# Kernel tuning notes

Measured on AMD Instinct MI355X. Metric: run time of the kernel, lower is better.

Reference implementation:

```python
import jax, jax.numpy as jnp
import numpy as np

ALPHA = 0.25
GAMMA = 2.0


def _calc_iou(a, b):
    # a: [A,4] anchors (y1,x1,y2,x2); b: [M,4] boxes (x1,y1,x2,y2)
    area = (b[:, 2] - b[:, 0]) * (b[:, 3] - b[:, 1])  # [M]
    iw = jnp.minimum(a[:, 3, None], b[None, :, 2]) - jnp.maximum(a[:, 1, None], b[None, :, 0])
    ih = jnp.minimum(a[:, 2, None], b[None, :, 3]) - jnp.maximum(a[:, 0, None], b[None, :, 1])
    iw = jnp.maximum(iw, 0.0)
    ih = jnp.maximum(ih, 0.0)
    ua = ((a[:, 2] - a[:, 0]) * (a[:, 3] - a[:, 1]))[:, None] + area[None, :] - iw * ih
    ua = jnp.maximum(ua, 1e-8)
    return iw * ih / ua  # [A,M]


def _detection_loss(classification, regression, annot, anchor):
    aw = anchor[:, 3] - anchor[:, 1]
    ah = anchor[:, 2] - anchor[:, 0]
    acx = anchor[:, 1] + 0.5 * aw
    acy = anchor[:, 0] + 0.5 * ah

    valid = annot[:, 4] != -1  # [M]; setup guarantees >=1 valid per image
    p = jnp.clip(classification, 1e-4, 1.0 - 1e-4)

    iou = jnp.where(valid[None, :], _calc_iou(anchor, annot[:, :4]), -1.0)  # [A,M]
    iou_max = iou.max(axis=1)
    iou_arg = iou.argmax(axis=1)
    assigned = annot[iou_arg]  # [A,5]

    big = (assigned[:, 2] - assigned[:, 0]) * (assigned[:, 3] - assigned[:, 1]) > 100.0
    pos = jnp.where(big, iou_max >= 0.5, iou_max >= 0.15)  # [A] bool
    posf = pos.astype(p.dtype)
    num_pos = posf.sum()

    C = p.shape[1]
    targets = jax.nn.one_hot(assigned[:, 4].astype(jnp.int32), C, dtype=p.dtype) * posf[:, None]

    alpha_factor = jnp.where(targets == 1.0, ALPHA, 1.0 - ALPHA)
    focal_weight = jnp.where(targets == 1.0, 1.0 - p, p)
    bce = -(targets * jnp.log(p) + (1.0 - targets) * jnp.log(1.0 - p))
    cls_loss = (alpha_factor * focal_weight ** GAMMA * bce).sum() / jnp.maximum(num_pos, 1.0)

    gw = assigned[:, 2] - assigned[:, 0]
    gh = assigned[:, 3] - assigned[:, 1]
    gcx = assigned[:, 0] + 0.5 * gw
    gcy = assigned[:, 1] + 0.5 * gh
    gw = jnp.maximum(gw, 1.0)
    gh = jnp.maximum(gh, 1.0)
    tdx = (gcx - acx) / aw
    tdy = (gcy - acy) / ah
    tdw = jnp.log(gw / aw)
    tdh = jnp.log(gh / ah)
    tgt = jnp.stack([tdy, tdx, tdh, tdw], axis=1)  # [A,4]
    diff = jnp.abs(tgt - regression)
    rl = jnp.where(diff <= 1.0 / 9.0, 0.5 * 9.0 * diff ** 2, diff - 0.5 / 9.0)
    reg_loss = jnp.where(num_pos > 0,
                         (rl * posf[:, None]).sum() / (4.0 * jnp.maximum(num_pos, 1.0)),
                         jnp.zeros((), p.dtype))
    return cls_loss, reg_loss


def _tversky_loss(y_pred, y_true, alpha=0.7, beta=0.3, gamma=4.0 / 3.0):
    bs, C = y_pred.shape[0], y_pred.shape[1]
    yp = y_pred.reshape(bs, C, -1)
    yt = y_true.reshape(bs, C, -1)
    inter = (yp * yt).sum(axis=(0, 2))
    fp = (yp * (1.0 - yt)).sum(axis=(0, 2))
    fn = ((1.0 - yp) * yt).sum(axis=(0, 2))
    score = inter / jnp.maximum(inter + alpha * fp + beta * fn, 1e-7)
    mask = (yt.sum(axis=(0, 2)) > 0).astype(y_pred.dtype)
    loss = (1.0 - score) * mask
    return loss.mean() ** gamma


def _focal_seg_loss(logits, target, alpha=0.25, gamma=2.0):
    x = logits.reshape(-1)
    y = target.reshape(-1)
    logpt = jnp.logaddexp(0.0, x) - x * y  # BCE-with-logits, stable
    pt = jnp.exp(-logpt)
    loss = (1.0 - pt) ** gamma * logpt * (alpha * y + (1.0 - alpha) * (1.0 - y))
    return loss.mean()


def reference(classifications, regressions, anchors, annotations, segmentation, seg_annot):
    anchor = anchors[0]
    cls_l, reg_l = jax.vmap(lambda c, r, a: _detection_loss(c, r, a, anchor))(
        classifications, regressions, annotations)
    cls_loss = cls_l.mean(keepdims=True)
    reg_loss = reg_l.mean(keepdims=True) * 50.0
    seg_loss = _tversky_loss(segmentation, seg_annot) + _focal_seg_loss(segmentation, seg_annot)
    return cls_loss, reg_loss, seg_loss


def setup_inputs() -> dict:
    B, A, M, NV = 32, 46035, 64, 40
    H, W, SEGC = 384, 640, 3
    ks = jax.random.split(jax.random.key(0), 12)

    classifications = jax.random.uniform(ks[0], (B, A, 1), dtype=jnp.float32)
    regressions = jax.random.normal(ks[1], (B, A, 4), dtype=jnp.float32) * 0.1

    cx = jax.random.uniform(ks[2], (A,)) * W
    cy = jax.random.uniform(ks[3], (A,)) * H
    sw = jax.random.uniform(ks[4], (A,)) * 240.0 + 8.0
    sh = jax.random.uniform(ks[5], (A,)) * 240.0 + 8.0
    anchors = jnp.stack([cy - 0.5 * sh, cx - 0.5 * sw, cy + 0.5 * sh, cx + 0.5 * sw], axis=1)[None]

    x1 = jax.random.uniform(ks[6], (B, M)) * (W - 140.0)
    y1 = jax.random.uniform(ks[7], (B, M)) * (H - 140.0)
    bw = jax.random.uniform(ks[8], (B, M)) * 126.0 + 4.0
    bh = jax.random.uniform(ks[9], (B, M)) * 126.0 + 4.0
    boxes = jnp.stack([x1, y1, x1 + bw, y1 + bh, jnp.zeros((B, M))], axis=2)
    valid = (jnp.arange(M) < NV)[None, :, None]
    annotations = jnp.where(valid, boxes, -1.0).astype(jnp.float32)

    segmentation = jax.random.normal(ks[10], (B, SEGC, H, W), dtype=jnp.float32)
    labels = jax.random.randint(ks[11], (B, H, W), 0, SEGC)
    seg_annot = jnp.moveaxis(jax.nn.one_hot(labels, SEGC, dtype=jnp.float32), -1, 1)

    return {"classifications": classifications, "regressions": regressions,
            "anchors": anchors, "annotations": annotations,
            "segmentation": segmentation, "seg_annot": seg_annot}
```

## Files before the change

### kernel.cpp

```cpp
#include <hip/hip_runtime.h>
#include <math.h>

#define A_N 46035
#define B_N 32
#define M_N 64
#define SEGC 3
#define HW 245760
#define HW4 61440
#define NBP 60
#define SEG_BLOCKS (B_N * SEGC * NBP)
#define SEG_TOTAL 23592960
#define DET_K 4
#define ABLK 45
#define DET_BLOCKS (ABLK * B_N)
#define F4_PER_BLOCK (HW4 / NBP)
#define F4_PER_THREAD 4

#define DET_WS (3 * B_N * ABLK)
#define SEG_WS_OFF DET_WS
#define SEG_S (B_N * NBP)

__device__ __forceinline__ double waveRed(double v) {
    for (int o = 32; o; o >>= 1) v += __shfl_down(v, o, 64);
    return v;
}

__device__ __forceinline__ void det_path(
    int blk, const float* __restrict__ cls, const float* __restrict__ reg,
    const float* __restrict__ anc, const float* __restrict__ ann,
    double* __restrict__ ws)
{
    const int b = blk / ABLK;
    const int bx = blk % ABLK;
    const int tid = threadIdx.x;
    const int a_base = bx * (256 * DET_K) + tid;

    __shared__ float4 sbox[M_N];
    __shared__ float2 sal[M_N];
    __shared__ int smv;
    if (tid < M_N) {
        const float* p = &ann[(b * M_N + tid) * 5];
        const float x1 = p[0], y1 = p[1], x2 = p[2], y2 = p[3], lb = p[4];
        sbox[tid] = make_float4(x1, y1, x2, y2);
        sal[tid] = make_float2((x2 - x1) * (y2 - y1), lb);
        unsigned long long vm = __ballot(lb != -1.0f);
        if (tid == 0) smv = (int)__popcll(vm);
    }
    __syncthreads();
    const int mv = smv;

    float ax1[DET_K], ay1[DET_K], ax2[DET_K], ay2[DET_K], aarea[DET_K];
    float binter[DET_K], bua[DET_K], pc[DET_K];
    int barg[DET_K];

    #pragma unroll
    for (int k = 0; k < DET_K; ++k) {
        const int a = a_base + k * 256;
        const int al = (a < A_N) ? a : (A_N - 1);
        const float4 av = *reinterpret_cast<const float4*>(&anc[al * 4]);
        ay1[k] = av.x; ax1[k] = av.y; ay2[k] = av.z; ax2[k] = av.w;
        aarea[k] = (av.z - av.x) * (av.w - av.y);
        binter[k] = -1.0f;
        bua[k] = 1.0f;
        barg[k] = 0;
        pc[k] = cls[b * A_N + al];
    }

    #pragma unroll 4
    for (int m = 0; m < mv; ++m) {
        const float4 bb = sbox[m];
        const float ba = sal[m].x;
        #pragma unroll
        for (int k = 0; k < DET_K; ++k) {
            const float iw = fmaxf(fminf(ax2[k], bb.z) - fmaxf(ax1[k], bb.x), 0.0f);
            const float ih = fmaxf(fminf(ay2[k], bb.w) - fmaxf(ay1[k], bb.y), 0.0f);
            const float inter = iw * ih;
            const float ua = (aarea[k] + ba) - inter;
            const bool upd = inter * bua[k] > binter[k] * ua;
            binter[k] = upd ? inter : binter[k];
            bua[k]    = upd ? ua    : bua[k];
            barg[k]   = upd ? m     : barg[k];
        }
    }

    float cls_f = 0.0f, reg_f = 0.0f;
    int pos_i = 0;

    #pragma unroll
    for (int k = 0; k < DET_K; ++k) {
        const int a = a_base + k * 256;
        if (a >= A_N) continue;
        const float4 g = sbox[barg[k]];
        const float2 al2 = sal[barg[k]];

        const bool big = al2.x > 100.0f;
        const float thr = big ? 0.5f : 0.15f;
        const bool pos = binter[k] >= thr * bua[k];
        pos_i += pos ? 1 : 0;

        float p = pc[k];
        p = fminf(fmaxf(p, 1e-4f), 1.0f - 1e-4f);
        const bool t1 = pos && ((int)al2.y == 0);
        const float af = t1 ? 0.25f : 0.75f;
        const float fw = t1 ? (1.0f - p) : p;
        const float bce = t1 ? (-logf(p)) : (-logf(1.0f - p));
        cls_f += af * fw * fw * bce;

        if (pos) {
            const float aw = ax2[k] - ax1[k];
            const float ah = ay2[k] - ay1[k];
            const float acx = ax1[k] + 0.5f * aw;
            const float acy = ay1[k] + 0.5f * ah;
            const float gw0 = g.z - g.x;
            const float gh0 = g.w - g.y;
            const float gcx = g.x + 0.5f * gw0;
            const float gcy = g.y + 0.5f * gh0;
            const float gw = fmaxf(gw0, 1.0f);
            const float gh = fmaxf(gh0, 1.0f);
            const float t0 = (gcy - acy) / ah;
            const float t1r = (gcx - acx) / aw;
            const float t2 = logf(gh / ah);
            const float t3 = logf(gw / aw);

            const float4 rv = *reinterpret_cast<const float4*>(&reg[(size_t)(b * A_N + a) * 4]);
            float d, rl, s = 0.0f;
            d = fabsf(t0 - rv.x);  rl = (d <= 1.0f/9.0f) ? 4.5f*d*d : d - 0.5f/9.0f; s += rl;
            d = fabsf(t1r - rv.y); rl = (d <= 1.0f/9.0f) ? 4.5f*d*d : d - 0.5f/9.0f; s += rl;
            d = fabsf(t2 - rv.z);  rl = (d <= 1.0f/9.0f) ? 4.5f*d*d : d - 0.5f/9.0f; s += rl;
            d = fabsf(t3 - rv.w);  rl = (d <= 1.0f/9.0f) ? 4.5f*d*d : d - 0.5f/9.0f; s += rl;
            reg_f += s;
        }
    }

    double cls_c = (double)cls_f, reg_c = (double)reg_f, pos_c = (double)pos_i;

    __shared__ double sredd[3][4];
    const int wid = threadIdx.x >> 6, lane = threadIdx.x & 63;
    cls_c = waveRed(cls_c);
    reg_c = waveRed(reg_c);
    pos_c = waveRed(pos_c);
    if (lane == 0) { sredd[0][wid] = cls_c; sredd[1][wid] = reg_c; sredd[2][wid] = pos_c; }
    __syncthreads();
    if (threadIdx.x == 0) {
        double c = 0, r = 0, pp = 0;
        for (int w = 0; w < 4; ++w) { c += sredd[0][w]; r += sredd[1][w]; pp += sredd[2][w]; }
        ws[0 * (B_N * ABLK) + b * ABLK + bx] = c;
        ws[1 * (B_N * ABLK) + b * ABLK + bx] = r;
        ws[2 * (B_N * ABLK) + b * ABLK + bx] = pp;
    }
}

__device__ __forceinline__ void seg_path(
    int sblk, const float* __restrict__ pred, const float* __restrict__ annot,
    double* __restrict__ ws)
{
    const int plane = sblk / NBP;
    const int bp = sblk % NBP;
    const int c = plane % SEGC;
    const int im = plane / SEGC;
    const long base4 = (long)plane * HW4 + (long)bp * F4_PER_BLOCK;

    const float4* __restrict__ p4 = reinterpret_cast<const float4*>(pred);
    const float4* __restrict__ t4 = reinterpret_cast<const float4*>(annot);

    float4 P[F4_PER_THREAD], T[F4_PER_THREAD];
    #pragma unroll
    for (int j = 0; j < F4_PER_THREAD; ++j) {
        const long idx = base4 + (long)(j * 256 + threadIdx.x);
        P[j] = p4[idx];
        T[j] = t4[idx];
    }
    __builtin_amdgcn_sched_barrier(0);

    float sxy = 0.0f, sx = 0.0f, syv = 0.0f, foc = 0.0f;
    #pragma unroll
    for (int j = 0; j < F4_PER_THREAD; ++j) {
        const float px[4] = { P[j].x, P[j].y, P[j].z, P[j].w };
        const float tx[4] = { T[j].x, T[j].y, T[j].z, T[j].w };
        #pragma unroll
        for (int e = 0; e < 4; ++e) {
            const float x = px[e], y = tx[e];
            const bool sel = y > 0.5f;
            sxy = fmaf(x, y, sxy);
            sx += x;
            syv += y;
            const float s = sel ? x : -x;
            const float t = __expf(-s);
            const float u = 1.0f + t;
            const float r = __builtin_amdgcn_rcpf(u);
            const float omp = t * r;
            const float logpt = __logf(u);
            const float w = fmaf(y, -0.5f, 0.75f);
            foc = fmaf(omp * omp * logpt, w, foc);
        }
    }

    double inter = (double)sxy, sxd = (double)sx, ycv = (double)syv, fo = (double)foc;

    __shared__ double sreds[4][4];
    const int wid = threadIdx.x >> 6, lane = threadIdx.x & 63;
    inter = waveRed(inter);
    sxd   = waveRed(sxd);
    ycv   = waveRed(ycv);
    fo    = waveRed(fo);
    if (lane == 0) { sreds[0][wid] = inter; sreds[1][wid] = sxd; sreds[2][wid] = ycv; sreds[3][wid] = fo; }
    __syncthreads();
    if (threadIdx.x == 0) {
        double a = 0, b2 = 0, cc = 0, dd = 0;
        for (int w = 0; w < 4; ++w) { a += sreds[0][w]; b2 += sreds[1][w]; cc += sreds[2][w]; dd += sreds[3][w]; }
        const int s = im * NBP + bp;
        double* seg_ws = ws + SEG_WS_OFF;
        seg_ws[(c * 4 + 0) * SEG_S + s] = a;
        seg_ws[(c * 4 + 1) * SEG_S + s] = b2;
        seg_ws[(c * 4 + 2) * SEG_S + s] = cc;
        seg_ws[(c * 4 + 3) * SEG_S + s] = dd;
    }
}

__global__ __launch_bounds__(256) void fused_kernel(
    const float* __restrict__ cls, const float* __restrict__ reg,
    const float* __restrict__ anc, const float* __restrict__ ann,
    const float* __restrict__ pred, const float* __restrict__ annot,
    double* __restrict__ ws)
{
    const int blk = blockIdx.x;
    if (blk % 5 == 0) {
        det_path(blk / 5, cls, reg, anc, ann, ws);
    } else {
        seg_path(blk - 1 - blk / 5, pred, annot, ws);
    }
}

__global__ __launch_bounds__(1024) void fin_kernel(
    const double* __restrict__ ws, float* __restrict__ out)
{
    __shared__ double sseg[SEGC][4];
    __shared__ double sdet[3][B_N];

    const int t = threadIdx.x;

    if (t < 768) {
        const int w = t >> 6, lane = t & 63;
        const int c = w >> 2, q = w & 3;
        const double* base = ws + SEG_WS_OFF + (c * 4 + q) * SEG_S;
        double s = 0.0;
        #pragma unroll
        for (int i = 0; i < SEG_S / 64; ++i)
            s += base[i * 64 + lane];
        s = waveRed(s);
        if (lane == 0) sseg[c][q] = s;
    } else if (t < 768 + 96) {
        const int r = t - 768;
        const int q = r >> 5, b = r & 31;
        const double* base = ws + q * (B_N * ABLK) + b * ABLK;
        double s = 0.0;
        #pragma unroll
        for (int i = 0; i < ABLK; ++i) s += base[i];
        sdet[q][b] = s;
    }
    __syncthreads();

    if (t == 0) {
        double clsm = 0.0, regm = 0.0;
        for (int b = 0; b < B_N; ++b) {
            const double np_ = sdet[2][b];
            const double mnp = fmax(np_, 1.0);
            clsm += sdet[0][b] / mnp;
            regm += (np_ > 0.0) ? sdet[1][b] / (4.0 * mnp) : 0.0;
        }
        clsm /= (double)B_N;
        regm = regm / (double)B_N * 50.0;

        double tsum = 0.0;
        for (int c = 0; c < SEGC; ++c) {
            const double inter = sseg[c][0];
            const double fpv = sseg[c][1] - inter;
            const double ycnt = sseg[c][2];
            const double fnv = ycnt - inter;
            const double denom = fmax(inter + 0.7 * fpv + 0.3 * fnv, 1e-7);
            const double score = inter / denom;
            const double mask = (ycnt > 0.0) ? 1.0 : 0.0;
            tsum += (1.0 - score) * mask;
        }
        const double tv = pow(tsum / 3.0, 4.0 / 3.0);
        double focm = 0.0;
        for (int c = 0; c < SEGC; ++c) focm += sseg[c][3];
        focm /= (double)SEG_TOTAL;

        out[0] = (float)clsm;
        out[1] = (float)regm;
        out[2] = (float)(tv + focm);
    }
}

extern "C" void kernel_launch(void* const* d_in, const int* in_sizes, int n_in,
                              void* d_out, int out_size, void* d_ws, size_t ws_size,
                              hipStream_t stream) {
    const float* cls    = (const float*)d_in[0];
    const float* reg    = (const float*)d_in[1];
    const float* anc    = (const float*)d_in[2];
    const float* ann    = (const float*)d_in[3];
    const float* seg    = (const float*)d_in[4];
    const float* segann = (const float*)d_in[5];
    double* ws = (double*)d_ws;
    float* out = (float*)d_out;

    fused_kernel<<<DET_BLOCKS + SEG_BLOCKS, 256, 0, stream>>>(
        cls, reg, anc, ann, seg, segann, ws);
    fin_kernel<<<1, 1024, 0, stream>>>(ws, out);
}
```

Baseline: 76.77 us.

## Rebalance fused det/seg block split and use fast log/rcp intrinsics

Halves segmentation blocks per plane (each thread now handles two batches of four float4 loads) and doubles detection blocks (two anchors per thread instead of four). Detection and segmentation blocks now alternate one-to-one instead of one-in-five, so the two kinds of work are interleaved more evenly across the grid. It also swaps logf and divisions in the detection path for __logf and hardware reciprocal. The aim is better load balance and less per-thread latency in the detection path, at the cost of slight precision loss and a different workspace layout that the finalize kernel reads.

```diff
diff --git a/kernel.cpp b/kernel.cpp
--- a/kernel.cpp
+++ b/kernel.cpp
@@ -7,14 +7,13 @@
 #define SEGC 3
 #define HW 245760
 #define HW4 61440
-#define NBP 60
+#define NBP 30
 #define SEG_BLOCKS (B_N * SEGC * NBP)
 #define SEG_TOTAL 23592960
-#define DET_K 4
-#define ABLK 45
+#define DET_K 2
+#define ABLK 90
 #define DET_BLOCKS (ABLK * B_N)
 #define F4_PER_BLOCK (HW4 / NBP)
-#define F4_PER_THREAD 4
 
 #define DET_WS (3 * B_N * ABLK)
 #define SEG_WS_OFF DET_WS
@@ -103,7 +102,7 @@
         const bool t1 = pos && ((int)al2.y == 0);
         const float af = t1 ? 0.25f : 0.75f;
         const float fw = t1 ? (1.0f - p) : p;
-        const float bce = t1 ? (-logf(p)) : (-logf(1.0f - p));
+        const float bce = t1 ? (-__logf(p)) : (-__logf(1.0f - p));
         cls_f += af * fw * fw * bce;
 
         if (pos) {
@@ -117,10 +116,12 @@
             const float gcy = g.y + 0.5f * gh0;
             const float gw = fmaxf(gw0, 1.0f);
             const float gh = fmaxf(gh0, 1.0f);
-            const float t0 = (gcy - acy) / ah;
-            const float t1r = (gcx - acx) / aw;
-            const float t2 = logf(gh / ah);
-            const float t3 = logf(gw / aw);
+            const float rah = __builtin_amdgcn_rcpf(ah);
+            const float raw = __builtin_amdgcn_rcpf(aw);
+            const float t0 = (gcy - acy) * rah;
+            const float t1r = (gcx - acx) * raw;
+            const float t2 = __logf(gh * rah);
+            const float t3 = __logf(gw * raw);
 
             const float4 rv = *reinterpret_cast<const float4*>(&reg[(size_t)(b * A_N + a) * 4]);
             float d, rl, s = 0.0f;
@@ -163,35 +164,37 @@
     const float4* __restrict__ p4 = reinterpret_cast<const float4*>(pred);
     const float4* __restrict__ t4 = reinterpret_cast<const float4*>(annot);
 
-    float4 P[F4_PER_THREAD], T[F4_PER_THREAD];
-    #pragma unroll
-    for (int j = 0; j < F4_PER_THREAD; ++j) {
-        const long idx = base4 + (long)(j * 256 + threadIdx.x);
-        P[j] = p4[idx];
-        T[j] = t4[idx];
-    }
-    __builtin_amdgcn_sched_barrier(0);
-
     float sxy = 0.0f, sx = 0.0f, syv = 0.0f, foc = 0.0f;
-    #pragma unroll
-    for (int j = 0; j < F4_PER_THREAD; ++j) {
-        const float px[4] = { P[j].x, P[j].y, P[j].z, P[j].w };
-        const float tx[4] = { T[j].x, T[j].y, T[j].z, T[j].w };
+
+    for (int it = 0; it < 2; ++it) {
+        float4 P[4], T[4];
         #pragma unroll
-        for (int e = 0; e < 4; ++e) {
-            const float x = px[e], y = tx[e];
-            const bool sel = y > 0.5f;
-            sxy = fmaf(x, y, sxy);
-            sx += x;
-            syv += y;
-            const float s = sel ? x : -x;
-            const float t = __expf(-s);
-            const float u = 1.0f + t;
-            const float r = __builtin_amdgcn_rcpf(u);
-            const float omp = t * r;
-            const float logpt = __logf(u);
-            const float w = fmaf(y, -0.5f, 0.75f);
-            foc = fmaf(omp * omp * logpt, w, foc);
+        for (int j = 0; j < 4; ++j) {
+            const long idx = base4 + (long)(it * 1024 + j * 256 + threadIdx.x);
+            P[j] = p4[idx];
+            T[j] = t4[idx];
+        }
+        __builtin_amdgcn_sched_barrier(0);
+        #pragma unroll
+        for (int j = 0; j < 4; ++j) {
+            const float px[4] = { P[j].x, P[j].y, P[j].z, P[j].w };
+            const float tx[4] = { T[j].x, T[j].y, T[j].z, T[j].w };
+            #pragma unroll
+            for (int e = 0; e < 4; ++e) {
+                const float x = px[e], y = tx[e];
+                const bool sel = y > 0.5f;
+                sxy = fmaf(x, y, sxy);
+                sx += x;
+                syv += y;
+                const float s = sel ? x : -x;
+                const float t = __expf(-s);
+                const float u = 1.0f + t;
+                const float r = __builtin_amdgcn_rcpf(u);
+                const float omp = t * r;
+                const float logpt = __logf(u);
+                const float w = fmaf(y, -0.5f, 0.75f);
+                foc = fmaf(omp * omp * logpt, w, foc);
+            }
         }
     }
 
@@ -224,10 +227,10 @@
     double* __restrict__ ws)
 {
     const int blk = blockIdx.x;
-    if (blk % 5 == 0) {
-        det_path(blk / 5, cls, reg, anc, ann, ws);
+    if ((blk & 1) == 0) {
+        det_path(blk >> 1, cls, reg, anc, ann, ws);
     } else {
-        seg_path(blk - 1 - blk / 5, pred, annot, ws);
+        seg_path(blk >> 1, pred, annot, ws);
     }
 }
 
@@ -254,7 +257,6 @@
         const int q = r >> 5, b = r & 31;
         const double* base = ws + q * (B_N * ABLK) + b * ABLK;
         double s = 0.0;
-        #pragma unroll
         for (int i = 0; i < ABLK; ++i) s += base[i];
         sdet[q][b] = s;
     }
```

Result: faster. 70.68 us (-7.9%).
